# Optimization experiments

Measured on AMD Instinct MI355X. Metric: run time of the kernel, lower is better.

Reference implementation:

```python
import jax, jax.numpy as jnp
import numpy as np

H_HEADS = 16
STATE_N = 64

def setup_inputs() -> dict:
    key = jax.random.key(0)
    ks = jax.random.split(key, 9)
    B, T, D = 2, 1024, 1024
    H, ch, N = H_HEADS, D // H_HEADS, STATE_N
    inp = jax.random.normal(ks[0], (B, T, D), dtype=jnp.float32)
    # lin_logA params scaled so exp(cumsum(logA)) stays bounded (decaying state)
    W_logA = jax.random.normal(ks[1], (H, 1, ch), dtype=jnp.float32) * 0.01
    b_logA = jnp.full((H, 1), -0.05, dtype=jnp.float32)
    W_XBC = jax.random.normal(ks[3], (H, ch + 2 * N, ch), dtype=jnp.float32) * (1.0 / np.sqrt(ch))
    b_XBC = jax.random.normal(ks[4], (H, ch + 2 * N), dtype=jnp.float32) * 0.02
    W_gate = jax.random.normal(ks[5], (H, ch, ch), dtype=jnp.float32) * (1.0 / np.sqrt(ch))
    b_gate = jax.random.normal(ks[6], (H, ch), dtype=jnp.float32) * 0.02
    W_out = jax.random.normal(ks[7], (D, D), dtype=jnp.float32) * (1.0 / np.sqrt(D))
    b_out = jax.random.normal(ks[8], (D,), dtype=jnp.float32) * 0.02
    return {"inp": inp, "W_logA": W_logA, "b_logA": b_logA, "W_XBC": W_XBC,
            "b_XBC": b_XBC, "W_gate": W_gate, "b_gate": b_gate,
            "W_out": W_out, "b_out": b_out}

def _mamba2_forward(inp, W_logA, b_logA, W_XBC, b_XBC, W_gate, b_gate, W_out, b_out):
    B, T, D = inp.shape
    H, N = H_HEADS, STATE_N
    ch = D // H
    x = inp.reshape(B, T, H, ch)  # B,T,H,ch
    # MultiheadLinear: matmul((H,out,in), x[...,None]) + bias
    logA = jnp.einsum('hoc,bthc->btho', W_logA, x)[..., 0] + b_logA[:, 0]  # B,T,H
    XBC = jax.nn.silu(jnp.einsum('hoc,bthc->btho', W_XBC, x) + b_XBC)     # B,T,H,ch+2N
    X = XBC[..., :ch]                 # B,T,H,ch
    Bm = XBC[..., ch:ch + N]          # B,T,H,N
    Cm = XBC[..., ch + N:]            # B,T,H,N
    # quadratic SSM: A_ss[b,h,i,j] = exp(cum[i]-cum[j]) for j<=i else 0
    cum = jnp.cumsum(jnp.swapaxes(logA, 1, 2), axis=-1)  # B,H,T
    diff = cum[..., :, None] - cum[..., None, :]          # B,H,T,T
    causal = jnp.tril(jnp.ones((T, T), dtype=bool))
    A_ss = jnp.where(causal, jnp.exp(jnp.where(causal, diff, 0.0)), 0.0)  # B,H,T,T
    G = jnp.einsum('bihn,bjhn->bhij', Cm, Bm)             # B,H,T,T (C_i . B_j)
    Y = jnp.einsum('bhij,bjhc->bihc', A_ss * G, X)        # B,T,H,ch
    gate = jnp.einsum('hoc,bthc->btho', W_gate, x) + b_gate
    Yg = (gate * Y).reshape(B, T, D)
    return Yg @ W_out.T + b_out

def reference(inp, W_logA, b_logA, W_XBC, b_XBC, W_gate, b_gate, W_out, b_out):
    return _mamba2_forward(inp, W_logA, b_logA, W_XBC, b_XBC, W_gate, b_gate, W_out, b_out)
```

## Files before the change

### kernel.cpp

```cpp
#include <hip/hip_runtime.h>

typedef unsigned int   u32;
typedef unsigned short u16;
typedef __attribute__((ext_vector_type(8))) short bf16x8;
typedef __attribute__((ext_vector_type(4))) float f32x4;

__device__ __forceinline__ float bfs(u16 u) {
  union { u32 i; float f; } v; v.i = ((u32)u) << 16; return v.f;
}
__device__ __forceinline__ u16 f2bf(float f) {
  union { float f; u32 i; } v; v.f = f;
  u32 r = v.i + 0x7fffu + ((v.i >> 16) & 1u);
  return (u16)(r >> 16);
}
__device__ __forceinline__ ushort4 f2bf4(float4 v) {
  ushort4 p; p.x = f2bf(v.x); p.y = f2bf(v.y); p.z = f2bf(v.z); p.w = f2bf(v.w);
  return p;
}

__global__ __launch_bounds__(256) void k_proj(
    const float* __restrict__ inp,
    const float* __restrict__ W_XBC,  const float* __restrict__ b_XBC,
    const float* __restrict__ W_gate, const float* __restrict__ b_gate,
    const float* __restrict__ W_logA, const float* __restrict__ b_logA,
    u16* __restrict__ XsT, u16* __restrict__ Bms, u16* __restrict__ BmsT,
    u16* __restrict__ Cms, u16* __restrict__ gates, float* __restrict__ logAs)
{
  int tt = blockIdx.x, h = blockIdx.y;
  int tid = threadIdx.x;
  int w = tid >> 6, l = tid & 63, q = l >> 4, lr = l & 15;
  int m0 = tt * 64;
  int b = m0 >> 10, tl0 = m0 & 1023;
  int bh = b * 16 + h;

  __shared__ u16 Xt[64][72];
  __shared__ u16 Wt[256][72];
  __shared__ float wl[64];

  if (tid < 64) wl[tid] = W_logA[h * 64 + tid];
#pragma unroll
  for (int i = 0; i < 4; ++i) {
    int f = tid + 256 * i; int r = f >> 4, cq = f & 15;
    float4 xv = *(const float4*)(inp + (size_t)(m0 + r) * 1024 + h * 64 + 4 * cq);
    *(ushort4*)&Xt[r][4 * cq] = f2bf4(xv);
  }
#pragma unroll
  for (int i = 0; i < 16; ++i) {
    int f = tid + 256 * i; int r = f >> 4, cq = f & 15;
    const float* wsrc = (r < 192) ? (W_XBC + ((size_t)h * 192 + r) * 64)
                                  : (W_gate + ((size_t)h * 64 + (r - 192)) * 64);
    *(ushort4*)&Wt[r][4 * cq] = f2bf4(*(const float4*)(wsrc + 4 * cq));
  }
  __syncthreads();

  bf16x8 af[4][2];
#pragma unroll
  for (int rt = 0; rt < 4; ++rt) {
    af[rt][0] = *(const bf16x8*)&Xt[16 * rt + lr][q * 8];
    af[rt][1] = *(const bf16x8*)&Xt[16 * rt + lr][32 + q * 8];
  }

  f32x4 acc[4][4];
#pragma unroll
  for (int rt = 0; rt < 4; ++rt)
#pragma unroll
    for (int ct = 0; ct < 4; ++ct) acc[rt][ct] = (f32x4){0.f, 0.f, 0.f, 0.f};

#pragma unroll
  for (int ct = 0; ct < 4; ++ct) {
    bf16x8 b0 = *(const bf16x8*)&Wt[64 * w + 16 * ct + lr][q * 8];
    bf16x8 b1 = *(const bf16x8*)&Wt[64 * w + 16 * ct + lr][32 + q * 8];
#pragma unroll
    for (int rt = 0; rt < 4; ++rt) {
      acc[rt][ct] = __builtin_amdgcn_mfma_f32_16x16x32_bf16(af[rt][0], b0, acc[rt][ct], 0, 0, 0);
      acc[rt][ct] = __builtin_amdgcn_mfma_f32_16x16x32_bf16(af[rt][1], b1, acc[rt][ct], 0, 0, 0);
    }
  }

  if (tid < 64) {
    float a = b_logA[h];
#pragma unroll 16
    for (int k = 0; k < 64; ++k) a += bfs(Xt[tid][k]) * wl[k];
    logAs[(size_t)bh * 1024 + tl0 + tid] = a;
  }

  if (w == 0) {
#pragma unroll
    for (int ct = 0; ct < 4; ++ct) {
      int n = 16 * ct + lr;
      float bias = b_XBC[h * 192 + n];
#pragma unroll
      for (int rt = 0; rt < 4; ++rt) {
        float4 v;
#pragma unroll
        for (int r = 0; r < 4; ++r) {
          float s = acc[rt][ct][r] + bias;
          (&v.x)[r] = s / (1.f + __expf(-s));
        }
        *(ushort4*)(XsT + ((size_t)bh * 64 + n) * 1024 + tl0 + 16 * rt + q * 4) = f2bf4(v);
      }
    }
  } else if (w == 1) {
#pragma unroll
    for (int ct = 0; ct < 4; ++ct) {
      int n = 16 * ct + lr;
      float bias = b_XBC[h * 192 + 64 + n];
#pragma unroll
      for (int rt = 0; rt < 4; ++rt) {
        float4 v;
#pragma unroll
        for (int r = 0; r < 4; ++r) {
          float s = acc[rt][ct][r] + bias;
          (&v.x)[r] = s / (1.f + __expf(-s));
        }
        ushort4 pv = f2bf4(v);
        *(ushort4*)(BmsT + ((size_t)bh * 64 + n) * 1024 + tl0 + 16 * rt + q * 4) = pv;
        u16 vs[4] = {pv.x, pv.y, pv.z, pv.w};
#pragma unroll
        for (int r = 0; r < 4; ++r) {
          int tloc = tl0 + 16 * rt + q * 4 + r;
          Bms[((size_t)bh * 1024 + tloc) * 64 + n] = vs[r];
        }
      }
    }
  } else if (w == 2) {
#pragma unroll
    for (int ct = 0; ct < 4; ++ct) {
      int n = 16 * ct + lr;
      float bias = b_XBC[h * 192 + 128 + n];
#pragma unroll
      for (int rt = 0; rt < 4; ++rt)
#pragma unroll
        for (int r = 0; r < 4; ++r) {
          int tloc = tl0 + 16 * rt + q * 4 + r;
          float s = acc[rt][ct][r] + bias;
          s = s / (1.f + __expf(-s));
          Cms[((size_t)bh * 1024 + tloc) * 64 + n] = f2bf(s);
        }
    }
  } else {
#pragma unroll
    for (int ct = 0; ct < 4; ++ct) {
      int n = 16 * ct + lr;
      float bias = b_gate[h * 64 + n];
#pragma unroll
      for (int rt = 0; rt < 4; ++rt)
#pragma unroll
        for (int r = 0; r < 4; ++r) {
          int tg = m0 + 16 * rt + q * 4 + r;
          gates[((size_t)tg * 16 + h) * 64 + n] = f2bf(acc[rt][ct][r] + bias);
        }
    }
  }
}

__global__ __launch_bounds__(1024) void k_scan(
    const float* __restrict__ logAs, float* __restrict__ rowexp,
    float* __restrict__ colexp,
    const float* __restrict__ Wout, u16* __restrict__ WoutB)
{
  int bh = blockIdx.x;
  int t = threadIdx.x;
  int wv = t >> 6, ln = t & 63;
  __shared__ float wsum[16];
  float v = logAs[(size_t)bh * 1024 + t];
#pragma unroll
  for (int off = 1; off < 64; off <<= 1) {
    float n = __shfl_up(v, off, 64);
    if (ln >= off) v += n;
  }
  if (ln == 63) wsum[wv] = v;
  __syncthreads();
  if (wv == 0) {
    float s = (ln < 16) ? wsum[ln] : 0.f;
#pragma unroll
    for (int off = 1; off < 16; off <<= 1) {
      float n = __shfl_up(s, off, 64);
      if (ln >= off) s += n;
    }
    if (ln < 16) wsum[ln] = s;
  }
  __syncthreads();
  if (wv > 0) v += wsum[wv - 1];
  rowexp[(size_t)bh * 1024 + t] = __expf(v);
  colexp[(size_t)bh * 1024 + t] = __expf(-v);

  int gtid = bh * 1024 + t;
#pragma unroll
  for (int i = 0; i < 8; ++i) {
    int idx = gtid + 32768 * i;
    float4 wv4 = ((const float4*)Wout)[idx];
    ((ushort4*)WoutB)[idx] = f2bf4(wv4);
  }
}

__global__ __launch_bounds__(256) void k_state(
    const u16* __restrict__ XsT, const u16* __restrict__ BmsT,
    const float* __restrict__ colexp, float* __restrict__ G)
{
  int jt = blockIdx.x, bh = blockIdx.y;
  int tid = threadIdx.x;
  int w = tid >> 6, l = tid & 63, q = l >> 4, lr = l & 15;
  int j0 = jt * 64;

  __shared__ u16 Bt[64][72];
  __shared__ u16 Xt[64][72];

#pragma unroll
  for (int i = 0; i < 4; ++i) {
    int f = tid + 256 * i; int r = f >> 4, cq = f & 15;
    *(ushort4*)&Bt[r][4 * cq] =
        *(const ushort4*)(BmsT + ((size_t)bh * 64 + r) * 1024 + j0 + 4 * cq);
    ushort4 xv = *(const ushort4*)(XsT + ((size_t)bh * 64 + r) * 1024 + j0 + 4 * cq);
    float4 ce = *(const float4*)(colexp + (size_t)bh * 1024 + j0 + 4 * cq);
    float4 sv;
    sv.x = bfs(xv.x) * ce.x; sv.y = bfs(xv.y) * ce.y;
    sv.z = bfs(xv.z) * ce.z; sv.w = bfs(xv.w) * ce.w;
    *(ushort4*)&Xt[r][4 * cq] = f2bf4(sv);
  }
  __syncthreads();

  bf16x8 a0 = *(const bf16x8*)&Bt[16 * w + lr][q * 8];
  bf16x8 a1 = *(const bf16x8*)&Bt[16 * w + lr][32 + q * 8];

  f32x4 acc[4];
#pragma unroll
  for (int ct = 0; ct < 4; ++ct) acc[ct] = (f32x4){0.f, 0.f, 0.f, 0.f};
#pragma unroll
  for (int ct = 0; ct < 4; ++ct) {
    bf16x8 b0 = *(const bf16x8*)&Xt[16 * ct + lr][q * 8];
    bf16x8 b1 = *(const bf16x8*)&Xt[16 * ct + lr][32 + q * 8];
    acc[ct] = __builtin_amdgcn_mfma_f32_16x16x32_bf16(a0, b0, acc[ct], 0, 0, 0);
    acc[ct] = __builtin_amdgcn_mfma_f32_16x16x32_bf16(a1, b1, acc[ct], 0, 0, 0);
  }

  float* Gt = G + ((size_t)bh * 16 + jt) * 4096;
#pragma unroll
  for (int ct = 0; ct < 4; ++ct)
#pragma unroll
    for (int r = 0; r < 4; ++r)
      Gt[(16 * w + q * 4 + r) * 64 + 16 * ct + lr] = acc[ct][r];
}

__global__ __launch_bounds__(1024) void k_prefix(
    const float* __restrict__ G, u16* __restrict__ HpreT)
{
  int bh = blockIdx.x;
  int tid = threadIdx.x;
  __shared__ float buf[64][65];
  float h[4] = {0.f, 0.f, 0.f, 0.f};
  for (int it = 0; it < 16; ++it) {
    size_t base = ((size_t)bh * 16 + it) * 4096;
#pragma unroll
    for (int k = 0; k < 4; ++k) {
      int e = tid + 1024 * k;
      buf[e >> 6][e & 63] = h[k];
    }
    __syncthreads();
#pragma unroll
    for (int k = 0; k < 4; ++k) {
      int e = tid + 1024 * k;
      int c = e >> 6, n = e & 63;
      HpreT[base + e] = f2bf(buf[n][c]);
      h[k] += G[base + e];
    }
    __syncthreads();
  }
}

__global__ __launch_bounds__(256) void k_ssm2(
    const u16* __restrict__ XsT, const u16* __restrict__ Bms, const u16* __restrict__ Cms,
    const float* __restrict__ rowexp, const float* __restrict__ colexp,
    const u16* __restrict__ HpreT, const u16* __restrict__ gates, u16* __restrict__ Yg)
{
  int it = blockIdx.x, bh = blockIdx.y;
  int b = bh >> 4, h = bh & 15;
  int tid = threadIdx.x;
  int w = tid >> 6, l = tid & 63, q = l >> 4, lr = l & 15;
  int i0 = it * 64;

  __shared__ u16 Cts[64][72];
  __shared__ u16 Bts[64][72];
  __shared__ u16 Xts[64][72];
  __shared__ u16 Sts[64][72];
  __shared__ u16 HTt[64][72];
  __shared__ float ref_[64], cef[64];

  const u16* Cb = Cms + (size_t)bh * 1024 * 64;
  const u16* Bb = Bms + (size_t)bh * 1024 * 64;
  const u16* Xb = XsT + (size_t)bh * 64 * 1024;
  const u16* Hb = HpreT + ((size_t)bh * 16 + it) * 4096;

#pragma unroll
  for (int i = 0; i < 4; ++i) {
    int f = tid + 256 * i; int r = f >> 4, cq = f & 15;
    *(ushort4*)&Cts[r][4 * cq] = *(const ushort4*)(Cb + (size_t)(i0 + r) * 64 + 4 * cq);
    *(ushort4*)&Bts[r][4 * cq] = *(const ushort4*)(Bb + (size_t)(i0 + r) * 64 + 4 * cq);
    *(ushort4*)&Xts[r][4 * cq] = *(const ushort4*)(Xb + (size_t)r * 1024 + i0 + 4 * cq);
    *(ushort4*)&HTt[r][4 * cq] = *(const ushort4*)(Hb + r * 64 + 4 * cq);
  }
  if (tid < 64) {
    ref_[tid] = rowexp[(size_t)bh * 1024 + i0 + tid];
    cef[tid]  = colexp[(size_t)bh * 1024 + i0 + tid];
  }
  __syncthreads();

  bf16x8 ca0 = *(const bf16x8*)&Cts[16 * w + lr][q * 8];
  bf16x8 ca1 = *(const bf16x8*)&Cts[16 * w + lr][32 + q * 8];

#pragma unroll
  for (int ct = 0; ct < 4; ++ct) {
    f32x4 s = (f32x4){0.f, 0.f, 0.f, 0.f};
    bf16x8 b0 = *(const bf16x8*)&Bts[16 * ct + lr][q * 8];
    bf16x8 b1 = *(const bf16x8*)&Bts[16 * ct + lr][32 + q * 8];
    s = __builtin_amdgcn_mfma_f32_16x16x32_bf16(ca0, b0, s, 0, 0, 0);
    s = __builtin_amdgcn_mfma_f32_16x16x32_bf16(ca1, b1, s, 0, 0, 0);
    int jl = 16 * ct + lr;
    float cj = cef[jl];
#pragma unroll
    for (int r = 0; r < 4; ++r) {
      int il = 16 * w + q * 4 + r;
      float v = (jl > il) ? 0.f : s[r] * ref_[il] * cj;
      Sts[il][jl] = f2bf(v);
    }
  }

  bf16x8 sa0 = *(const bf16x8*)&Sts[16 * w + lr][q * 8];
  bf16x8 sa1 = *(const bf16x8*)&Sts[16 * w + lr][32 + q * 8];
  f32x4 accd[4], acco[4];
#pragma unroll
  for (int ct = 0; ct < 4; ++ct) {
    accd[ct] = (f32x4){0.f, 0.f, 0.f, 0.f};
    acco[ct] = (f32x4){0.f, 0.f, 0.f, 0.f};
    bf16x8 x0 = *(const bf16x8*)&Xts[16 * ct + lr][q * 8];
    bf16x8 x1 = *(const bf16x8*)&Xts[16 * ct + lr][32 + q * 8];
    accd[ct] = __builtin_amdgcn_mfma_f32_16x16x32_bf16(sa0, x0, accd[ct], 0, 0, 0);
    accd[ct] = __builtin_amdgcn_mfma_f32_16x16x32_bf16(sa1, x1, accd[ct], 0, 0, 0);
    bf16x8 h0 = *(const bf16x8*)&HTt[16 * ct + lr][q * 8];
    bf16x8 h1 = *(const bf16x8*)&HTt[16 * ct + lr][32 + q * 8];
    acco[ct] = __builtin_amdgcn_mfma_f32_16x16x32_bf16(ca0, h0, acco[ct], 0, 0, 0);
    acco[ct] = __builtin_amdgcn_mfma_f32_16x16x32_bf16(ca1, h1, acco[ct], 0, 0, 0);
  }

#pragma unroll
  for (int ct = 0; ct < 4; ++ct) {
    int c = 16 * ct + lr;
#pragma unroll
    for (int r = 0; r < 4; ++r) {
      int il = 16 * w + q * 4 + r;
      int tg = i0 + il;
      size_t row = (size_t)(b * 1024 + tg);
      float y = accd[ct][r] + ref_[il] * acco[ct][r];
      float gt = bfs(gates[(row * 16 + h) * 64 + c]);
      Yg[row * 1024 + h * 64 + c] = f2bf(y * gt);
    }
  }
}

__global__ __launch_bounds__(512) void k_out(
    const u16* __restrict__ Yg, const u16* __restrict__ WoutB,
    const float* __restrict__ bout, float* __restrict__ out)
{
  int bm = blockIdx.x, bn = blockIdx.y;
  int tid = threadIdx.x;
  int w = tid >> 6, l = tid & 63, q = l >> 4, lr = l & 15;
  int m0 = bm * 128, d0 = bn * 64;

  __shared__ u16 Yt[128][72];
  __shared__ u16 Wt[64][72];

  f32x4 acc[4];
#pragma unroll
  for (int ct = 0; ct < 4; ++ct) acc[ct] = (f32x4){0.f, 0.f, 0.f, 0.f};

  ushort4 py[4], pw[2];
#pragma unroll
  for (int i = 0; i < 4; ++i) {
    int f = tid + 512 * i; int r = f >> 4, cq = f & 15;
    py[i] = *(const ushort4*)(Yg + (size_t)(m0 + r) * 1024 + 4 * cq);
  }
#pragma unroll
  for (int i = 0; i < 2; ++i) {
    int f = tid + 512 * i; int r = f >> 4, cq = f & 15;
    pw[i] = *(const ushort4*)(WoutB + (size_t)(d0 + r) * 1024 + 4 * cq);
  }

  for (int kt = 0; kt < 16; ++kt) {
    __syncthreads();
#pragma unroll
    for (int i = 0; i < 4; ++i) {
      int f = tid + 512 * i; int r = f >> 4, cq = f & 15;
      *(ushort4*)&Yt[r][4 * cq] = py[i];
    }
#pragma unroll
    for (int i = 0; i < 2; ++i) {
      int f = tid + 512 * i; int r = f >> 4, cq = f & 15;
      *(ushort4*)&Wt[r][4 * cq] = pw[i];
    }
    __syncthreads();

    if (kt < 15) {
      int k1 = (kt + 1) * 64;
#pragma unroll
      for (int i = 0; i < 4; ++i) {
        int f = tid + 512 * i; int r = f >> 4, cq = f & 15;
        py[i] = *(const ushort4*)(Yg + (size_t)(m0 + r) * 1024 + k1 + 4 * cq);
      }
#pragma unroll
      for (int i = 0; i < 2; ++i) {
        int f = tid + 512 * i; int r = f >> 4, cq = f & 15;
        pw[i] = *(const ushort4*)(WoutB + (size_t)(d0 + r) * 1024 + k1 + 4 * cq);
      }
    }

    bf16x8 a0 = *(const bf16x8*)&Yt[16 * w + lr][q * 8];
    bf16x8 a1 = *(const bf16x8*)&Yt[16 * w + lr][32 + q * 8];
#pragma unroll
    for (int ct = 0; ct < 4; ++ct) {
      bf16x8 b0 = *(const bf16x8*)&Wt[16 * ct + lr][q * 8];
      bf16x8 b1 = *(const bf16x8*)&Wt[16 * ct + lr][32 + q * 8];
      acc[ct] = __builtin_amdgcn_mfma_f32_16x16x32_bf16(a0, b0, acc[ct], 0, 0, 0);
      acc[ct] = __builtin_amdgcn_mfma_f32_16x16x32_bf16(a1, b1, acc[ct], 0, 0, 0);
    }
  }

#pragma unroll
  for (int ct = 0; ct < 4; ++ct) {
    int d = d0 + 16 * ct + lr;
    float bo = bout[d];
#pragma unroll
    for (int r = 0; r < 4; ++r) {
      int m = m0 + 16 * w + q * 4 + r;
      out[(size_t)m * 1024 + d] = acc[ct][r] + bo;
    }
  }
}

extern "C" void kernel_launch(void* const* d_in, const int* in_sizes, int n_in,
                              void* d_out, int out_size, void* d_ws, size_t ws_size,
                              hipStream_t stream)
{
  const float* inp   = (const float*)d_in[0];
  const float* WlogA = (const float*)d_in[1];
  const float* blogA = (const float*)d_in[2];
  const float* WXBC  = (const float*)d_in[3];
  const float* bXBC  = (const float*)d_in[4];
  const float* Wgate = (const float*)d_in[5];
  const float* bgate = (const float*)d_in[6];
  const float* Wout  = (const float*)d_in[7];
  const float* bout  = (const float*)d_in[8];
  float* out = (float*)d_out;

  const size_t SZ = (size_t)2 * 16 * 1024 * 64;
  float* logAs  = (float*)d_ws;
  float* rowexp = logAs + 32768;
  float* colexp = rowexp + 32768;
  float* G      = colexp + 32768;
  u16* base16  = (u16*)(G + (size_t)32 * 16 * 4096);
  u16* XsT   = base16;
  u16* Bms   = XsT + SZ;
  u16* BmsT  = Bms + SZ;
  u16* Cms   = BmsT + SZ;
  u16* gates = Cms + SZ;
  u16* Yg    = gates + SZ;
  u16* WoutB = Yg + SZ;
  u16* HpreT = WoutB + 1024 * 1024;

  k_proj<<<dim3(32, 16), 256, 0, stream>>>(inp, WXBC, bXBC, Wgate, bgate,
                                           WlogA, blogA, XsT, Bms, BmsT, Cms,
                                           gates, logAs);
  k_scan<<<32, 1024, 0, stream>>>(logAs, rowexp, colexp, Wout, WoutB);
  k_state<<<dim3(16, 32), 256, 0, stream>>>(XsT, BmsT, colexp, G);
  k_prefix<<<32, 1024, 0, stream>>>(G, HpreT);
  k_ssm2<<<dim3(16, 32), 256, 0, stream>>>(XsT, Bms, Cms, rowexp, colexp,
                                           HpreT, gates, Yg);
  k_out<<<dim3(16, 16), 512, 0, stream>>>(Yg, WoutB, bout, out);
}
```

Baseline: 128.4 us.

## Fuse scan, chunk-state GEMM and prefix sum into one kernel; pre-convert weights

Merges the cumsum scan, per-chunk state GEMM and chunk prefix accumulation into a single 32-block kernel that keeps chunk states in shared memory as bf16, removing the fp32 G round trip through global memory and two launches. A separate prep kernel converts the XBC, gate and output weights to bf16 once, so the projection kernel no longer re-converts weights in each of its 32 token-tile blocks. In exchange, the state GEMM now runs on only 32 blocks instead of 512, and partial states are rounded to bf16 before the prefix sum, which adds precision loss.

```diff
diff --git a/kernel.cpp b/kernel.cpp
--- a/kernel.cpp
+++ b/kernel.cpp
@@ -18,10 +18,27 @@
   return p;
 }
 
+__global__ __launch_bounds__(256) void k_prep(
+    const float* __restrict__ WXBC, const float* __restrict__ Wgate,
+    const float* __restrict__ Wout,
+    u16* __restrict__ WXBCb, u16* __restrict__ Wgateb, u16* __restrict__ WoutB)
+{
+  int i = blockIdx.x * 256 + threadIdx.x;
+  if (i < 49152) {
+    ((ushort4*)WXBCb)[i] = f2bf4(((const float4*)WXBC)[i]);
+  } else if (i < 65536) {
+    int j = i - 49152;
+    ((ushort4*)Wgateb)[j] = f2bf4(((const float4*)Wgate)[j]);
+  } else {
+    int j = i - 65536;
+    ((ushort4*)WoutB)[j] = f2bf4(((const float4*)Wout)[j]);
+  }
+}
+
 __global__ __launch_bounds__(256) void k_proj(
     const float* __restrict__ inp,
-    const float* __restrict__ W_XBC,  const float* __restrict__ b_XBC,
-    const float* __restrict__ W_gate, const float* __restrict__ b_gate,
+    const u16* __restrict__ WXBCb,  const float* __restrict__ b_XBC,
+    const u16* __restrict__ Wgateb, const float* __restrict__ b_gate,
     const float* __restrict__ W_logA, const float* __restrict__ b_logA,
     u16* __restrict__ XsT, u16* __restrict__ Bms, u16* __restrict__ BmsT,
     u16* __restrict__ Cms, u16* __restrict__ gates, float* __restrict__ logAs)
@@ -47,9 +64,9 @@
 #pragma unroll
   for (int i = 0; i < 16; ++i) {
     int f = tid + 256 * i; int r = f >> 4, cq = f & 15;
-    const float* wsrc = (r < 192) ? (W_XBC + ((size_t)h * 192 + r) * 64)
-                                  : (W_gate + ((size_t)h * 64 + (r - 192)) * 64);
-    *(ushort4*)&Wt[r][4 * cq] = f2bf4(*(const float4*)(wsrc + 4 * cq));
+    const u16* ws = (r < 192) ? (WXBCb + ((size_t)h * 192 + r) * 64)
+                              : (Wgateb + ((size_t)h * 64 + (r - 192)) * 64);
+    *(ushort4*)&Wt[r][4 * cq] = *(const ushort4*)(ws + 4 * cq);
   }
   __syncthreads();
 
@@ -154,15 +171,21 @@
   }
 }
 
-__global__ __launch_bounds__(1024) void k_scan(
-    const float* __restrict__ logAs, float* __restrict__ rowexp,
-    float* __restrict__ colexp,
-    const float* __restrict__ Wout, u16* __restrict__ WoutB)
+__global__ __launch_bounds__(1024) void k_mid(
+    const float* __restrict__ logAs,
+    const u16* __restrict__ XsT, const u16* __restrict__ BmsT,
+    float* __restrict__ rowexp, float* __restrict__ colexp,
+    u16* __restrict__ HpreT)
 {
   int bh = blockIdx.x;
   int t = threadIdx.x;
   int wv = t >> 6, ln = t & 63;
+  int q = ln >> 4, lr = ln & 15;
+
   __shared__ float wsum[16];
+  __shared__ float cl[1024];
+  __shared__ u16 Lb[16][16][72];
+
   float v = logAs[(size_t)bh * 1024 + t];
 #pragma unroll
   for (int off = 1; off < 64; off <<= 1) {
@@ -182,89 +205,62 @@
   }
   __syncthreads();
   if (wv > 0) v += wsum[wv - 1];
+  float ce = __expf(-v);
   rowexp[(size_t)bh * 1024 + t] = __expf(v);
-  colexp[(size_t)bh * 1024 + t] = __expf(-v);
-
-  int gtid = bh * 1024 + t;
-#pragma unroll
-  for (int i = 0; i < 8; ++i) {
-    int idx = gtid + 32768 * i;
-    float4 wv4 = ((const float4*)Wout)[idx];
-    ((ushort4*)WoutB)[idx] = f2bf4(wv4);
-  }
-}
-
-__global__ __launch_bounds__(256) void k_state(
-    const u16* __restrict__ XsT, const u16* __restrict__ BmsT,
-    const float* __restrict__ colexp, float* __restrict__ G)
-{
-  int jt = blockIdx.x, bh = blockIdx.y;
-  int tid = threadIdx.x;
-  int w = tid >> 6, l = tid & 63, q = l >> 4, lr = l & 15;
-  int j0 = jt * 64;
-
-  __shared__ u16 Bt[64][72];
-  __shared__ u16 Xt[64][72];
-
-#pragma unroll
-  for (int i = 0; i < 4; ++i) {
-    int f = tid + 256 * i; int r = f >> 4, cq = f & 15;
-    *(ushort4*)&Bt[r][4 * cq] =
-        *(const ushort4*)(BmsT + ((size_t)bh * 64 + r) * 1024 + j0 + 4 * cq);
-    ushort4 xv = *(const ushort4*)(XsT + ((size_t)bh * 64 + r) * 1024 + j0 + 4 * cq);
-    float4 ce = *(const float4*)(colexp + (size_t)bh * 1024 + j0 + 4 * cq);
-    float4 sv;
-    sv.x = bfs(xv.x) * ce.x; sv.y = bfs(xv.y) * ce.y;
-    sv.z = bfs(xv.z) * ce.z; sv.w = bfs(xv.w) * ce.w;
-    *(ushort4*)&Xt[r][4 * cq] = f2bf4(sv);
-  }
+  colexp[(size_t)bh * 1024 + t] = ce;
+  cl[t] = ce;
   __syncthreads();
 
-  bf16x8 a0 = *(const bf16x8*)&Bt[16 * w + lr][q * 8];
-  bf16x8 a1 = *(const bf16x8*)&Bt[16 * w + lr][32 + q * 8];
-
-  f32x4 acc[4];
-#pragma unroll
-  for (int ct = 0; ct < 4; ++ct) acc[ct] = (f32x4){0.f, 0.f, 0.f, 0.f};
-#pragma unroll
-  for (int ct = 0; ct < 4; ++ct) {
-    bf16x8 b0 = *(const bf16x8*)&Xt[16 * ct + lr][q * 8];
-    bf16x8 b1 = *(const bf16x8*)&Xt[16 * ct + lr][32 + q * 8];
-    acc[ct] = __builtin_amdgcn_mfma_f32_16x16x32_bf16(a0, b0, acc[ct], 0, 0, 0);
-    acc[ct] = __builtin_amdgcn_mfma_f32_16x16x32_bf16(a1, b1, acc[ct], 0, 0, 0);
-  }
-
-  float* Gt = G + ((size_t)bh * 16 + jt) * 4096;
-#pragma unroll
-  for (int ct = 0; ct < 4; ++ct)
-#pragma unroll
-    for (int r = 0; r < 4; ++r)
-      Gt[(16 * w + q * 4 + r) * 64 + 16 * ct + lr] = acc[ct][r];
-}
-
-__global__ __launch_bounds__(1024) void k_prefix(
-    const float* __restrict__ G, u16* __restrict__ HpreT)
-{
-  int bh = blockIdx.x;
-  int tid = threadIdx.x;
-  __shared__ float buf[64][65];
-  float h[4] = {0.f, 0.f, 0.f, 0.f};
-  for (int it = 0; it < 16; ++it) {
-    size_t base = ((size_t)bh * 16 + it) * 4096;
-#pragma unroll
-    for (int k = 0; k < 4; ++k) {
-      int e = tid + 1024 * k;
-      buf[e >> 6][e & 63] = h[k];
-    }
+  int j0 = wv * 64;
+  const u16* Bbase = BmsT + (size_t)bh * 64 * 1024;
+  const u16* Xbase = XsT + (size_t)bh * 64 * 1024;
+
+  f32x4 acc[4][4];
+#pragma unroll
+  for (int rt = 0; rt < 4; ++rt)
+#pragma unroll
+    for (int ct = 0; ct < 4; ++ct) acc[rt][ct] = (f32x4){0.f, 0.f, 0.f, 0.f};
+
+#pragma unroll
+  for (int ct = 0; ct < 4; ++ct) {
+    const u16* xr = Xbase + ((size_t)(16 * ct + lr)) * 1024 + j0;
+    bf16x8 x0 = *(const bf16x8*)(xr + q * 8);
+    bf16x8 x1 = *(const bf16x8*)(xr + 32 + q * 8);
+    bf16x8 b0, b1;
+#pragma unroll
+    for (int jj = 0; jj < 8; ++jj) {
+      b0[jj] = (short)f2bf(bfs((u16)x0[jj]) * cl[j0 + q * 8 + jj]);
+      b1[jj] = (short)f2bf(bfs((u16)x1[jj]) * cl[j0 + 32 + q * 8 + jj]);
+    }
+#pragma unroll
+    for (int rt = 0; rt < 4; ++rt) {
+      const u16* br = Bbase + ((size_t)(16 * rt + lr)) * 1024 + j0;
+      bf16x8 a0 = *(const bf16x8*)(br + q * 8);
+      bf16x8 a1 = *(const bf16x8*)(br + 32 + q * 8);
+      acc[rt][ct] = __builtin_amdgcn_mfma_f32_16x16x32_bf16(a0, b0, acc[rt][ct], 0, 0, 0);
+      acc[rt][ct] = __builtin_amdgcn_mfma_f32_16x16x32_bf16(a1, b1, acc[rt][ct], 0, 0, 0);
+    }
+  }
+
+  int l16 = t >> 6, pos = t & 63;
+#pragma unroll
+  for (int ct = 0; ct < 4; ++ct) {
     __syncthreads();
 #pragma unroll
-    for (int k = 0; k < 4; ++k) {
-      int e = tid + 1024 * k;
-      int c = e >> 6, n = e & 63;
-      HpreT[base + e] = f2bf(buf[n][c]);
-      h[k] += G[base + e];
+    for (int rt = 0; rt < 4; ++rt) {
+      ushort4 pv;
+      pv.x = f2bf(acc[rt][ct][0]); pv.y = f2bf(acc[rt][ct][1]);
+      pv.z = f2bf(acc[rt][ct][2]); pv.w = f2bf(acc[rt][ct][3]);
+      *(ushort4*)&Lb[wv][lr][16 * rt + q * 4] = pv;
     }
     __syncthreads();
+    float hsum = 0.f;
+    size_t gbase = (size_t)bh * 16 * 4096 + ct * 1024 + t;
+#pragma unroll
+    for (int jt = 0; jt < 16; ++jt) {
+      HpreT[gbase + (size_t)jt * 4096] = f2bf(hsum);
+      hsum += bfs(Lb[jt][l16][pos]);
+    }
   }
 }
 
@@ -455,23 +451,23 @@
   float* logAs  = (float*)d_ws;
   float* rowexp = logAs + 32768;
   float* colexp = rowexp + 32768;
-  float* G      = colexp + 32768;
-  u16* base16  = (u16*)(G + (size_t)32 * 16 * 4096);
-  u16* XsT   = base16;
-  u16* Bms   = XsT + SZ;
-  u16* BmsT  = Bms + SZ;
-  u16* Cms   = BmsT + SZ;
-  u16* gates = Cms + SZ;
-  u16* Yg    = gates + SZ;
-  u16* WoutB = Yg + SZ;
-  u16* HpreT = WoutB + 1024 * 1024;
-
-  k_proj<<<dim3(32, 16), 256, 0, stream>>>(inp, WXBC, bXBC, Wgate, bgate,
+  u16* base16  = (u16*)(colexp + 32768);
+  u16* XsT    = base16;
+  u16* Bms    = XsT + SZ;
+  u16* BmsT   = Bms + SZ;
+  u16* Cms    = BmsT + SZ;
+  u16* gates  = Cms + SZ;
+  u16* Yg     = gates + SZ;
+  u16* WoutB  = Yg + SZ;
+  u16* HpreT  = WoutB + 1024 * 1024;
+  u16* WXBCb  = HpreT + (size_t)32 * 16 * 4096;
+  u16* Wgateb = WXBCb + 196608;
+
+  k_prep<<<1280, 256, 0, stream>>>(WXBC, Wgate, Wout, WXBCb, Wgateb, WoutB);
+  k_proj<<<dim3(32, 16), 256, 0, stream>>>(inp, WXBCb, bXBC, Wgateb, bgate,
                                            WlogA, blogA, XsT, Bms, BmsT, Cms,
                                            gates, logAs);
-  k_scan<<<32, 1024, 0, stream>>>(logAs, rowexp, colexp, Wout, WoutB);
-  k_state<<<dim3(16, 32), 256, 0, stream>>>(XsT, BmsT, colexp, G);
-  k_prefix<<<32, 1024, 0, stream>>>(G, HpreT);
+  k_mid<<<32, 1024, 0, stream>>>(logAs, XsT, BmsT, rowexp, colexp, HpreT);
   k_ssm2<<<dim3(16, 32), 256, 0, stream>>>(XsT, Bms, Cms, rowexp, colexp,
                                            HpreT, gates, Yg);
   k_out<<<dim3(16, 16), 512, 0, stream>>>(Yg, WoutB, bout, out);
```

After: 127.6 us. Within noise of the previous version (-0.6%).
